# Optimization experiments

Hardware: AMD Instinct MI355X
Metric: run time of the kernel (lower is better)

## Reference

```python
import jax, jax.numpy as jnp
import numpy as np

B, SQ, SK = 2, 2048, 4096
D_STATE, D_LISTEN, D_PROJ, H = 512, 512, 512, 8


def setup_inputs() -> dict:
    key = jax.random.key(0)
    ks = jax.random.split(key, 9)
    s = 0.02
    return {
        "q": jax.random.normal(ks[0], (B, SQ, D_STATE), jnp.float32),
        "k": jax.random.normal(ks[1], (B, SK, D_LISTEN), jnp.float32),
        "mask": jax.random.randint(ks[2], (B, SK), 0, 2, jnp.int32),
        "Wq": jax.random.normal(ks[3], (D_STATE, D_PROJ), jnp.float32) * s,
        "bq": jnp.zeros((D_PROJ,), jnp.float32),
        "Wk": jax.random.normal(ks[4], (D_LISTEN, D_PROJ), jnp.float32) * s,
        "bk": jnp.zeros((D_PROJ,), jnp.float32),
        "Wv": jax.random.normal(ks[5], (D_LISTEN, D_PROJ), jnp.float32) * s,
        "bv": jnp.zeros((D_PROJ,), jnp.float32),
    }


def reference(q, k, mask, Wq, bq, Wk, bk, Wv, bv):
    # projections
    qp = q @ Wq + bq                      # [B, SQ, D]
    kp = k @ Wk + bk                      # [B, SK, D]
    vp = k @ Wv + bv                      # [B, SK, D]
    W = D_PROJ // H                        # head width
    qh = qp.reshape(B, SQ, H, W).transpose(0, 2, 1, 3)  # [B,H,SQ,W]
    kh = kp.reshape(B, SK, H, W).transpose(0, 2, 1, 3)  # [B,H,SK,W]
    vh = vp.reshape(B, SK, H, W).transpose(0, 2, 1, 3)  # [B,H,SK,W]
    scores = jnp.einsum("bhqw,bhkw->bhqk", qh, kh) / np.sqrt(W).astype(np.float32)
    m = mask[:, None, None, :].astype(jnp.float32)       # [B,1,1,SK]
    scores = scores - 10000.0 * (1.0 - m)
    attn = jax.nn.softmax(scores, axis=-1)               # dropout=0 (eval)
    h = jnp.einsum("bhqk,bhkw->bhqw", attn, vh)          # [B,H,SQ,W]
    h = h.transpose(0, 2, 1, 3).reshape(B, SQ, D_PROJ)
    return h
```

## Files before the change

### kernel.cpp

```cpp
#include <hip/hip_runtime.h>
#include <hip/hip_bf16.h>


typedef short  s16x8 __attribute__((ext_vector_type(8)));
typedef short  s16x4 __attribute__((ext_vector_type(4)));
typedef float  f32x4 __attribute__((ext_vector_type(4)));
typedef float  f32x16 __attribute__((ext_vector_type(16)));
typedef unsigned int u32;
typedef unsigned int u32x4 __attribute__((ext_vector_type(4)));

__device__ __forceinline__ unsigned short f2bf(float x) {
    return __builtin_bit_cast(unsigned short, __float2bfloat16(x));
}
__device__ __forceinline__ void gload16(const void* g, void* lds) {
    __builtin_amdgcn_global_load_lds(
        (const __attribute__((address_space(1))) unsigned int*)g,
        (__attribute__((address_space(3))) unsigned int*)lds, 16, 0, 0);
}
__device__ __forceinline__ u32 cvtpk(float lo, float hi) {
    u32 r;
    asm("v_cvt_pk_bf16_f32 %0, %1, %2" : "=v"(r) : "v"(lo), "v"(hi));
    return r;
}

__global__ __launch_bounds__(256) void prep(
    const float* __restrict__ q, const float* __restrict__ k,
    const float* __restrict__ Wq, const float* __restrict__ Wk,
    const float* __restrict__ Wv, const int* __restrict__ mask,
    unsigned short* __restrict__ qbf, unsigned short* __restrict__ kbf,
    unsigned short* __restrict__ wtq, unsigned short* __restrict__ wtk,
    unsigned short* __restrict__ wtv, int* __restrict__ cntb)
{
    __shared__ float T[64][65];
    const int bid = blockIdx.x;
    const int tid = threadIdx.x;
    if (bid < 3072) {
        const float* src = bid < 1024 ? q : k;
        unsigned short* dst = bid < 1024 ? qbf : kbf;
        int i = (bid < 1024 ? bid : bid - 1024) * 256 + tid;
        float4 a = reinterpret_cast<const float4*>(src)[2 * i];
        float4 b = reinterpret_cast<const float4*>(src)[2 * i + 1];
        s16x8 o;
        o[0] = (short)f2bf(a.x); o[1] = (short)f2bf(a.y);
        o[2] = (short)f2bf(a.z); o[3] = (short)f2bf(a.w);
        o[4] = (short)f2bf(b.x); o[5] = (short)f2bf(b.y);
        o[6] = (short)f2bf(b.z); o[7] = (short)f2bf(b.w);
        reinterpret_cast<s16x8*>(dst)[i] = o;
    } else if (bid < 3264) {
        int t = bid - 3072;
        int z = t >> 6;
        int tt = t & 63;
        const float* W = z == 0 ? Wq : z == 1 ? Wk : Wv;
        unsigned short* D = z == 0 ? wtq : z == 1 ? wtk : wtv;
        const int k0 = (tt >> 3) * 64, n0 = (tt & 7) * 64;
        const int r = tid >> 2, cq = tid & 3;
        #pragma unroll
        for (int p = 0; p < 4; ++p) {
            int c = (cq + 4 * p) * 4;
            float4 v = *reinterpret_cast<const float4*>(
                &W[(size_t)(k0 + r) * 512 + n0 + c]);
            T[c + 0][r] = v.x; T[c + 1][r] = v.y;
            T[c + 2][r] = v.z; T[c + 3][r] = v.w;
        }
        __syncthreads();
        #pragma unroll
        for (int p = 0; p < 4; ++p) {
            int kc = (cq + 4 * p) * 4;
            s16x4 o;
            o[0] = (short)f2bf(T[r][kc + 0]);
            o[1] = (short)f2bf(T[r][kc + 1]);
            o[2] = (short)f2bf(T[r][kc + 2]);
            o[3] = (short)f2bf(T[r][kc + 3]);
            *reinterpret_cast<s16x4*>(&D[(size_t)(n0 + r) * 512 + k0 + kc]) = o;
        }
    } else {
        __shared__ int red[4];
        int b = bid - 3264;
        int base = b * 4096 + tid * 16;
        int s = 0;
        #pragma unroll
        for (int p = 0; p < 4; ++p) {
            int4 m = *reinterpret_cast<const int4*>(&mask[base + 4 * p]);
            s += m.x + m.y + m.z + m.w;
        }
        #pragma unroll
        for (int off = 1; off < 64; off <<= 1)
            s += __shfl_xor(s, off);
        if ((tid & 63) == 0) red[tid >> 6] = s;
        __syncthreads();
        if (tid == 0)
            cntb[b] = 4096 - (red[0] + red[1] + red[2] + red[3]);
    }
}

__global__ __launch_bounds__(256) void proj4(
    const unsigned short* __restrict__ qbf, const unsigned short* __restrict__ kbf,
    const unsigned short* __restrict__ wtq, const unsigned short* __restrict__ wtk,
    const unsigned short* __restrict__ wtv,
    const float* __restrict__ bq, const float* __restrict__ bk,
    const float* __restrict__ bv, const int* __restrict__ mask,
    unsigned short* __restrict__ qh, unsigned short* __restrict__ kh,
    unsigned short* __restrict__ vt)
{
    __shared__ unsigned short As[2][128 * 64];
    __shared__ unsigned short Bs[2][128 * 64];

    const int tid  = threadIdx.x;
    const int wv   = tid >> 6;
    const int lane = tid & 63;
    const int g    = lane >> 4;
    const int ln   = lane & 15;
    const int swz  = (ln & 7) << 3;
    const int r0   = (wv >> 1) * 64;
    const int c0   = (wv & 1) * 64;

    const int id = blockIdx.x;
    const unsigned short *A, *Wt;
    const float* bias;
    unsigned short* dst;
    int S, trans, nb, mb, mflag;
    if (id < 128) {
        int local = id;
        A = qbf; Wt = wtq; bias = bq; dst = qh; S = 2048; trans = 0; mflag = 0;
        nb = local >> 5; mb = local & 31;
    } else if (id < 384) {
        int local = id - 128;
        A = kbf; Wt = wtk; bias = bk; dst = kh; S = 4096; trans = 0; mflag = 1;
        nb = local >> 6; mb = local & 63;
    } else {
        int local = id - 384;
        A = kbf; Wt = wtv; bias = bv; dst = vt; S = 4096; trans = 1; mflag = 2;
        nb = local >> 6; mb = local & 63;
    }
    const int m0 = mb * 128, n0 = nb * 128;
    const float scl = (mflag == 0) ? 0.18033688011112042f : 1.f;

    f32x4 acc[4][4];
    #pragma unroll
    for (int i = 0; i < 4; ++i)
        #pragma unroll
        for (int j = 0; j < 4; ++j) acc[i][j] = (f32x4)0.f;

    auto stage = [&](int bufn, int k0) {
        #pragma unroll
        for (int p = 0; p < 4; ++p) {
            int slot = p * 256 + tid;
            int row = slot >> 3, cb = slot & 7;
            int cbp = cb ^ (row & 7);
            gload16(&A[(size_t)(m0 + row) * 512 + k0 + cbp * 8], &As[bufn][slot * 8]);
        }
        #pragma unroll
        for (int p = 0; p < 4; ++p) {
            int slot = p * 256 + tid;
            int row = slot >> 3, cb = slot & 7;
            int cbp = cb ^ (row & 7);
            gload16(&Wt[(size_t)(n0 + row) * 512 + k0 + cbp * 8], &Bs[bufn][slot * 8]);
        }
    };

    stage(0, 0);
    __syncthreads();
    int buf = 0;
    for (int kk = 0; kk < 8; ++kk) {
        if (kk < 7) stage(buf ^ 1, (kk + 1) * 64);
        #pragma unroll
        for (int ks = 0; ks < 2; ++ks) {
            s16x8 fa[4], fb[4];
            #pragma unroll
            for (int mi = 0; mi < 4; ++mi)
                fa[mi] = *reinterpret_cast<const s16x8*>(
                    &As[buf][((r0 + 16 * mi + ln) * 64 + ks * 32 + g * 8) ^ swz]);
            #pragma unroll
            for (int nj = 0; nj < 4; ++nj)
                fb[nj] = *reinterpret_cast<const s16x8*>(
                    &Bs[buf][((c0 + 16 * nj + ln) * 64 + ks * 32 + g * 8) ^ swz]);
            if (!trans) {
                #pragma unroll
                for (int mi = 0; mi < 4; ++mi)
                    #pragma unroll
                    for (int nj = 0; nj < 4; ++nj)
                        acc[mi][nj] = __builtin_amdgcn_mfma_f32_16x16x32_bf16(
                            fa[mi], fb[nj], acc[mi][nj], 0, 0, 0);
            } else {
                #pragma unroll
                for (int mi = 0; mi < 4; ++mi)
                    #pragma unroll
                    for (int nj = 0; nj < 4; ++nj)
                        acc[mi][nj] = __builtin_amdgcn_mfma_f32_16x16x32_bf16(
                            fb[nj], fa[mi], acc[mi][nj], 0, 0, 0);
            }
        }
        __syncthreads();
        buf ^= 1;
    }

    const int head = nb * 2 + (c0 >> 6);
    const int bidx = m0 / S;
    const int s0   = m0 - bidx * S;

    if (!trans) {
        float bvv[4];
        #pragma unroll
        for (int nj = 0; nj < 4; ++nj) bvv[nj] = bias[n0 + c0 + 16 * nj + ln];
        unsigned short* base = dst + (size_t)(bidx * 8 + head) * S * 64;
        #pragma unroll
        for (int mi = 0; mi < 4; ++mi)
            #pragma unroll
            for (int r = 0; r < 4; ++r) {
                int s = s0 + r0 + 16 * mi + 4 * g + r;
                float fm = (mflag == 1) ? (float)mask[bidx * 4096 + s] : 1.f;
                float fs = fm * scl;
                #pragma unroll
                for (int nj = 0; nj < 4; ++nj)
                    base[(size_t)s * 64 + 16 * nj + ln] =
                        f2bf((acc[mi][nj][r] + bvv[nj]) * fs);
            }
    } else {
        float fmc[4];
        #pragma unroll
        for (int mi = 0; mi < 4; ++mi)
            fmc[mi] = (float)mask[bidx * 4096 + s0 + r0 + 16 * mi + ln];
        unsigned short* base = dst + (size_t)(bidx * 8 + head) * 64 * (size_t)S;
        #pragma unroll
        for (int nj = 0; nj < 4; ++nj)
            #pragma unroll
            for (int r = 0; r < 4; ++r) {
                int wl = 16 * nj + 4 * g + r;
                float bw = bias[n0 + c0 + wl];
                #pragma unroll
                for (int mi = 0; mi < 4; ++mi)
                    base[(size_t)wl * S + s0 + r0 + 16 * mi + ln] =
                        f2bf((acc[mi][nj][r] + bw) * fmc[mi]);
            }
    }
}

__global__ __launch_bounds__(512) void attn16(
    const unsigned short* __restrict__ qh,
    const unsigned short* __restrict__ kh,
    const unsigned short* __restrict__ vt,
    const int* __restrict__ cntb,
    float* __restrict__ out)
{
    __shared__ float Ored[2][4][32][36];
    __shared__ float lw[2][2][4][32];

    const int tid  = threadIdx.x;
    const int wid  = tid >> 6;
    const int kq   = wid & 3;
    const int qg   = wid >> 2;
    const int lane = tid & 63;
    const int l31  = lane & 31;
    const int h32  = lane >> 5;

    const int id  = blockIdx.x;
    const int xcd = id & 7;
    const int j   = id >> 3;
    const int bh  = xcd * 2 + (j >> 4);
    const int qt  = j & 15;
    const int b   = bh >> 3;
    const int hh  = bh & 7;

    const unsigned short* Kp = kh + (size_t)bh * 4096 * 64
                               + (size_t)(kq * 32 + l31) * 64 + h32 * 8;
    const unsigned short* Vp0 = vt + (size_t)bh * 64 * 4096
                               + (size_t)l31 * 4096 + kq * 32 + h32 * 8;

    s16x8 Qf[2][4];
    {
        const unsigned short* Qb = qh + ((size_t)bh * 2048 + qt * 128 + qg * 64) * 64;
        #pragma unroll
        for (int qt2 = 0; qt2 < 2; ++qt2)
            #pragma unroll
            for (int ks = 0; ks < 4; ++ks)
                Qf[qt2][ks] = *reinterpret_cast<const s16x8*>(
                    &Qb[(size_t)(qt2 * 32 + l31) * 64 + ks * 16 + h32 * 8]);
    }

    f32x16 O[2][2], Ol[2];
    #pragma unroll
    for (int i = 0; i < 2; ++i) {
        Ol[i] = (f32x16)0.f;
        #pragma unroll
        for (int jj = 0; jj < 2; ++jj) O[i][jj] = (f32x16)0.f;
    }

    s16x8 ones;
    #pragma unroll
    for (int i = 0; i < 8; ++i) ones[i] = (short)0x3F80;

    s16x8 kf[4], vf[4];

    auto loadK = [&](int t) {
        #pragma unroll
        for (int ks = 0; ks < 4; ++ks)
            kf[ks] = *reinterpret_cast<const s16x8*>(Kp + (size_t)t * 8192 + ks * 16);
    };
    auto loadV = [&](int t) {
        #pragma unroll
        for (int wt = 0; wt < 2; ++wt)
            #pragma unroll
            for (int t2 = 0; t2 < 2; ++t2)
                vf[wt * 2 + t2] = *reinterpret_cast<const s16x8*>(
                    Vp0 + (size_t)wt * 32 * 4096 + t * 128 + t2 * 16);
    };

    loadK(0); loadV(0);

    for (int t = 0; t < 32; ++t) {
        f32x16 S[2];
        S[0] = (f32x16)0.f; S[1] = (f32x16)0.f;
        __builtin_amdgcn_s_setprio(1);
        #pragma unroll
        for (int ks = 0; ks < 4; ++ks) {
            S[0] = __builtin_amdgcn_mfma_f32_32x32x16_bf16(kf[ks], Qf[0][ks], S[0], 0, 0, 0);
            S[1] = __builtin_amdgcn_mfma_f32_32x32x16_bf16(kf[ks], Qf[1][ks], S[1], 0, 0, 0);
        }
        __builtin_amdgcn_s_setprio(0);
        if (t < 31) loadK(t + 1);

        s16x8 pa[2][2];
        #pragma unroll
        for (int qt2 = 0; qt2 < 2; ++qt2) {
            float pp[16];
            #pragma unroll
            for (int r = 0; r < 16; ++r)
                pp[r] = exp2f(S[qt2][r]);
            u32 W[8];
            #pragma unroll
            for (int c = 0; c < 4; ++c) {
                W[2 * c + 0] = cvtpk(pp[4 * c + 0], pp[4 * c + 1]);
                W[2 * c + 1] = cvtpk(pp[4 * c + 2], pp[4 * c + 3]);
            }
            asm("v_permlane32_swap_b32 %0, %1" : "+v"(W[0]), "+v"(W[2]));
            asm("v_permlane32_swap_b32 %0, %1" : "+v"(W[1]), "+v"(W[3]));
            asm("v_permlane32_swap_b32 %0, %1" : "+v"(W[4]), "+v"(W[6]));
            asm("v_permlane32_swap_b32 %0, %1" : "+v"(W[5]), "+v"(W[7]));
            u32x4 lo, hi;
            lo[0] = W[0]; lo[1] = W[1]; lo[2] = W[2]; lo[3] = W[3];
            hi[0] = W[4]; hi[1] = W[5]; hi[2] = W[6]; hi[3] = W[7];
            pa[qt2][0] = __builtin_bit_cast(s16x8, lo);
            pa[qt2][1] = __builtin_bit_cast(s16x8, hi);
        }

        __builtin_amdgcn_s_setprio(1);
        #pragma unroll
        for (int qt2 = 0; qt2 < 2; ++qt2) {
            #pragma unroll
            for (int wt = 0; wt < 2; ++wt)
                #pragma unroll
                for (int t2 = 0; t2 < 2; ++t2)
                    O[qt2][wt] = __builtin_amdgcn_mfma_f32_32x32x16_bf16(
                        pa[qt2][t2], vf[wt * 2 + t2], O[qt2][wt], 0, 0, 0);
            #pragma unroll
            for (int t2 = 0; t2 < 2; ++t2)
                Ol[qt2] = __builtin_amdgcn_mfma_f32_32x32x16_bf16(
                    pa[qt2][t2], ones, Ol[qt2], 0, 0, 0);
        }
        __builtin_amdgcn_s_setprio(0);
        if (t < 31) loadV(t + 1);
    }

    if (l31 == 0) {
        #pragma unroll
        for (int qt2 = 0; qt2 < 2; ++qt2)
            #pragma unroll
            for (int r = 0; r < 16; ++r)
                lw[qg][qt2][kq][(r & 3) + 8 * (r >> 2) + 4 * h32] = Ol[qt2][r];
    }

    const float cnt = (float)cntb[b];
    const int grp = tid >> 8;
    const int tt  = tid & 255;
    const int qr  = tt >> 3;
    const int w8  = (tt & 7) * 4;
    #pragma unroll
    for (int qt2 = 0; qt2 < 2; ++qt2)
        #pragma unroll
        for (int wt = 0; wt < 2; ++wt) {
            __syncthreads();
            f32x16 oo = O[qt2][wt];
            #pragma unroll
            for (int r = 0; r < 16; ++r)
                Ored[qg][kq][(r & 3) + 8 * (r >> 2) + 4 * h32][l31] = oo[r];
            __syncthreads();
            float4 s  = *reinterpret_cast<const float4*>(&Ored[grp][0][qr][w8]);
            float4 s1 = *reinterpret_cast<const float4*>(&Ored[grp][1][qr][w8]);
            float4 s2 = *reinterpret_cast<const float4*>(&Ored[grp][2][qr][w8]);
            float4 s3 = *reinterpret_cast<const float4*>(&Ored[grp][3][qr][w8]);
            float l = (lw[grp][qt2][0][qr] + lw[grp][qt2][1][qr]
                     + lw[grp][qt2][2][qr] + lw[grp][qt2][3][qr]) - cnt;
            float inv = 1.f / l;
            int qglob = qt * 128 + grp * 64 + qt2 * 32 + qr;
            float4 o;
            o.x = (s.x + s1.x + s2.x + s3.x) * inv;
            o.y = (s.y + s1.y + s2.y + s3.y) * inv;
            o.z = (s.z + s1.z + s2.z + s3.z) * inv;
            o.w = (s.w + s1.w + s2.w + s3.w) * inv;
            *reinterpret_cast<float4*>(
                &out[((size_t)b * 2048 + qglob) * 512 + hh * 64 + wt * 32 + w8]) = o;
        }
}

extern "C" void kernel_launch(void* const* d_in, const int* in_sizes, int n_in,
                              void* d_out, int out_size, void* d_ws, size_t ws_size,
                              hipStream_t stream)
{
    const float* q    = (const float*)d_in[0];
    const float* k    = (const float*)d_in[1];
    const int*   mask = (const int*)  d_in[2];
    const float* Wq   = (const float*)d_in[3];
    const float* bq   = (const float*)d_in[4];
    const float* Wk   = (const float*)d_in[5];
    const float* bk   = (const float*)d_in[6];
    const float* Wv   = (const float*)d_in[7];
    const float* bv   = (const float*)d_in[8];
    float* out = (float*)d_out;

    unsigned short* p = (unsigned short*)d_ws;
    unsigned short* qh  = p; p += (size_t)2 * 8 * 2048 * 64;
    unsigned short* kh  = p; p += (size_t)2 * 8 * 4096 * 64;
    unsigned short* vt  = p; p += (size_t)2 * 8 * 4096 * 64;
    unsigned short* qbf = p; p += (size_t)2 * 2048 * 512;
    unsigned short* kbf = p; p += (size_t)2 * 4096 * 512;
    unsigned short* wtq = p; p += 512 * 512;
    unsigned short* wtk = p; p += 512 * 512;
    unsigned short* wtv = p; p += 512 * 512;
    int* cntb = (int*)p;

    dim3 blk(256);
    prep<<<dim3(3266), blk, 0, stream>>>(q, k, Wq, Wk, Wv, mask,
                                         qbf, kbf, wtq, wtk, wtv, cntb);
    proj4<<<dim3(640), blk, 0, stream>>>(qbf, kbf, wtq, wtk, wtv,
                                         bq, bk, bv, mask, qh, kh, vt);
    attn16<<<dim3(256), dim3(512), 0, stream>>>(qh, kh, vt, cntb, out);
}
```

Measured before the change: 95.87 us.

## Fuse fp32-to-bf16 activation conversion into projection GEMM staging

```diff
diff --git a/kernel.cpp b/kernel.cpp
--- a/kernel.cpp
+++ b/kernel.cpp
@@ -24,32 +24,17 @@
 }
 
 __global__ __launch_bounds__(256) void prep(
-    const float* __restrict__ q, const float* __restrict__ k,
     const float* __restrict__ Wq, const float* __restrict__ Wk,
     const float* __restrict__ Wv, const int* __restrict__ mask,
-    unsigned short* __restrict__ qbf, unsigned short* __restrict__ kbf,
     unsigned short* __restrict__ wtq, unsigned short* __restrict__ wtk,
     unsigned short* __restrict__ wtv, int* __restrict__ cntb)
 {
     __shared__ float T[64][65];
     const int bid = blockIdx.x;
     const int tid = threadIdx.x;
-    if (bid < 3072) {
-        const float* src = bid < 1024 ? q : k;
-        unsigned short* dst = bid < 1024 ? qbf : kbf;
-        int i = (bid < 1024 ? bid : bid - 1024) * 256 + tid;
-        float4 a = reinterpret_cast<const float4*>(src)[2 * i];
-        float4 b = reinterpret_cast<const float4*>(src)[2 * i + 1];
-        s16x8 o;
-        o[0] = (short)f2bf(a.x); o[1] = (short)f2bf(a.y);
-        o[2] = (short)f2bf(a.z); o[3] = (short)f2bf(a.w);
-        o[4] = (short)f2bf(b.x); o[5] = (short)f2bf(b.y);
-        o[6] = (short)f2bf(b.z); o[7] = (short)f2bf(b.w);
-        reinterpret_cast<s16x8*>(dst)[i] = o;
-    } else if (bid < 3264) {
-        int t = bid - 3072;
-        int z = t >> 6;
-        int tt = t & 63;
+    if (bid < 192) {
+        int z = bid >> 6;
+        int tt = bid & 63;
         const float* W = z == 0 ? Wq : z == 1 ? Wk : Wv;
         unsigned short* D = z == 0 ? wtq : z == 1 ? wtk : wtv;
         const int k0 = (tt >> 3) * 64, n0 = (tt & 7) * 64;
@@ -75,7 +60,7 @@
         }
     } else {
         __shared__ int red[4];
-        int b = bid - 3264;
+        int b = bid - 192;
         int base = b * 4096 + tid * 16;
         int s = 0;
         #pragma unroll
@@ -94,7 +79,7 @@
 }
 
 __global__ __launch_bounds__(256) void proj4(
-    const unsigned short* __restrict__ qbf, const unsigned short* __restrict__ kbf,
+    const float* __restrict__ qf, const float* __restrict__ kf2,
     const unsigned short* __restrict__ wtq, const unsigned short* __restrict__ wtk,
     const unsigned short* __restrict__ wtv,
     const float* __restrict__ bq, const float* __restrict__ bk,
@@ -115,21 +100,22 @@
     const int c0   = (wv & 1) * 64;
 
     const int id = blockIdx.x;
-    const unsigned short *A, *Wt;
+    const float* A;
+    const unsigned short* Wt;
     const float* bias;
     unsigned short* dst;
     int S, trans, nb, mb, mflag;
     if (id < 128) {
         int local = id;
-        A = qbf; Wt = wtq; bias = bq; dst = qh; S = 2048; trans = 0; mflag = 0;
+        A = qf; Wt = wtq; bias = bq; dst = qh; S = 2048; trans = 0; mflag = 0;
         nb = local >> 5; mb = local & 31;
     } else if (id < 384) {
         int local = id - 128;
-        A = kbf; Wt = wtk; bias = bk; dst = kh; S = 4096; trans = 0; mflag = 1;
+        A = kf2; Wt = wtk; bias = bk; dst = kh; S = 4096; trans = 0; mflag = 1;
         nb = local >> 6; mb = local & 63;
     } else {
         int local = id - 384;
-        A = kbf; Wt = wtv; bias = bv; dst = vt; S = 4096; trans = 1; mflag = 2;
+        A = kf2; Wt = wtv; bias = bv; dst = vt; S = 4096; trans = 1; mflag = 2;
         nb = local >> 6; mb = local & 63;
     }
     const int m0 = mb * 128, n0 = nb * 128;
@@ -141,14 +127,32 @@
         #pragma unroll
         for (int j = 0; j < 4; ++j) acc[i][j] = (f32x4)0.f;
 
-    auto stage = [&](int bufn, int k0) {
-        #pragma unroll
-        for (int p = 0; p < 4; ++p) {
-            int slot = p * 256 + tid;
-            int row = slot >> 3, cb = slot & 7;
+    float4 Ar[4][2];
+    auto issueA = [&](int k0) {
+        #pragma unroll
+        for (int p = 0; p < 4; ++p) {
+            int gslot = p * 256 + tid;
+            int row = gslot >> 3, cb = gslot & 7;
             int cbp = cb ^ (row & 7);
-            gload16(&A[(size_t)(m0 + row) * 512 + k0 + cbp * 8], &As[bufn][slot * 8]);
-        }
+            const float* src = &A[(size_t)(m0 + row) * 512 + k0 + cbp * 8];
+            Ar[p][0] = *reinterpret_cast<const float4*>(src);
+            Ar[p][1] = *reinterpret_cast<const float4*>(src + 4);
+        }
+    };
+    auto writeA = [&](int bufn) {
+        #pragma unroll
+        for (int p = 0; p < 4; ++p) {
+            int gslot = p * 256 + tid;
+            int row = gslot >> 3, cb = gslot & 7;
+            s16x8 o;
+            o[0] = (short)f2bf(Ar[p][0].x); o[1] = (short)f2bf(Ar[p][0].y);
+            o[2] = (short)f2bf(Ar[p][0].z); o[3] = (short)f2bf(Ar[p][0].w);
+            o[4] = (short)f2bf(Ar[p][1].x); o[5] = (short)f2bf(Ar[p][1].y);
+            o[6] = (short)f2bf(Ar[p][1].z); o[7] = (short)f2bf(Ar[p][1].w);
+            *reinterpret_cast<s16x8*>(&As[bufn][row * 64 + cb * 8]) = o;
+        }
+    };
+    auto stageW = [&](int bufn, int k0) {
         #pragma unroll
         for (int p = 0; p < 4; ++p) {
             int slot = p * 256 + tid;
@@ -158,11 +162,17 @@
         }
     };
 
-    stage(0, 0);
+    issueA(0);
+    stageW(0, 0);
+    writeA(0);
     __syncthreads();
+
     int buf = 0;
     for (int kk = 0; kk < 8; ++kk) {
-        if (kk < 7) stage(buf ^ 1, (kk + 1) * 64);
+        if (kk < 7) {
+            issueA((kk + 1) * 64);
+            stageW(buf ^ 1, (kk + 1) * 64);
+        }
         #pragma unroll
         for (int ks = 0; ks < 2; ++ks) {
             s16x8 fa[4], fb[4];
@@ -190,6 +200,7 @@
                             fb[nj], fa[mi], acc[mi][nj], 0, 0, 0);
             }
         }
+        if (kk < 7) writeA(buf ^ 1);
         __syncthreads();
         buf ^= 1;
     }
@@ -421,17 +432,15 @@
     unsigned short* qh  = p; p += (size_t)2 * 8 * 2048 * 64;
     unsigned short* kh  = p; p += (size_t)2 * 8 * 4096 * 64;
     unsigned short* vt  = p; p += (size_t)2 * 8 * 4096 * 64;
-    unsigned short* qbf = p; p += (size_t)2 * 2048 * 512;
-    unsigned short* kbf = p; p += (size_t)2 * 4096 * 512;
     unsigned short* wtq = p; p += 512 * 512;
     unsigned short* wtk = p; p += 512 * 512;
     unsigned short* wtv = p; p += 512 * 512;
     int* cntb = (int*)p;
 
     dim3 blk(256);
-    prep<<<dim3(3266), blk, 0, stream>>>(q, k, Wq, Wk, Wv, mask,
-                                         qbf, kbf, wtq, wtk, wtv, cntb);
-    proj4<<<dim3(640), blk, 0, stream>>>(qbf, kbf, wtq, wtk, wtv,
+    prep<<<dim3(194), blk, 0, stream>>>(Wq, Wk, Wv, mask,
+                                        wtq, wtk, wtv, cntb);
+    proj4<<<dim3(640), blk, 0, stream>>>(q, k, wtq, wtk, wtv,
                                          bq, bk, bv, mask, qh, kh, vt);
     attn16<<<dim3(256), dim3(512), 0, stream>>>(qh, kh, vt, cntb, out);
 }
```

After: 101.1 us. 1.06x slower.
